# Kernel optimization log

Hardware: AMD Instinct MI355X
Metric: run time of the kernel (lower is better)

The kernel has to match this reference:

```python
import jax, jax.numpy as jnp
import numpy as np

B, N_ATOMS, D = 4, 100000, 64
F, G, A = 8, 20000, 3
H = 16


def setup_inputs() -> dict:
    key = jax.random.key(0)
    k1, k2, k3, k4 = jax.random.split(key, 4)
    atoms_embeddings = jax.random.normal(k1, (B, N_ATOMS, D), dtype=jnp.float32)
    grounding_indices = jax.random.randint(k2, (F, G, A), 0, N_ATOMS, dtype=jnp.int64)
    # Glorot-ish scaling so sigmoids don't saturate
    W1 = jax.random.normal(k3, (F, A * D, H), dtype=jnp.float32) / np.sqrt(A * D)
    b1 = jnp.zeros((F, H), dtype=jnp.float32)
    W2 = jax.random.normal(k4, (F, H, 1), dtype=jnp.float32) / np.sqrt(H)
    b2 = jnp.zeros((F, 1), dtype=jnp.float32)
    return {
        "atoms_embeddings": atoms_embeddings,
        "grounding_indices": grounding_indices,
        "W1": W1, "b1": b1, "W2": W2, "b2": b2,
    }


def reference(atoms_embeddings, grounding_indices, W1, b1, W2, b2):
    # Gather clique atom embeddings: [B, F, G, A, D]
    gathered = jnp.take(atoms_embeddings, grounding_indices, axis=1)
    # Fuse atoms of each clique: [B, F, G, A*D]
    Bsz = atoms_embeddings.shape[0]
    x = gathered.reshape(Bsz, F, G, A * gathered.shape[-1])
    # Per-formula 2-layer sigmoid MLP (dropout is identity in inference)
    h = jax.nn.sigmoid(jnp.einsum('bfgk,fkh->bfgh', x, W1) + b1[None, :, None, :])
    o = jax.nn.sigmoid(jnp.einsum('bfgh,fho->bfgo', h, W2) + b2[None, :, None, :])
    # Squeeze last dim and concat formulas along last axis: [B, F*G]
    return o[..., 0].reshape(Bsz, F * G)
```

## Files before the change

kernel.cpp:

```cpp
#include <hip/hip_runtime.h>

#define B_      4
#define N_ATOMS 100000
#define D_      64
#define F_      8
#define G_      20000
#define A_      3
#define H_      16
#define AD_     (A_ * D_)
#define BLOCK   256
#define GPB     64
#define BSTRIDE ((size_t)N_ATOMS * D_)

#define FMA16(x1, wr)                                            \
    {                                                            \
        const float4 w0 = (wr)[0], w1v = (wr)[1],                \
                     w2v = (wr)[2], w3v = (wr)[3];               \
        h[0]  = fmaf((x1), w0.x,  h[0]);                         \
        h[1]  = fmaf((x1), w0.y,  h[1]);                         \
        h[2]  = fmaf((x1), w0.z,  h[2]);                         \
        h[3]  = fmaf((x1), w0.w,  h[3]);                         \
        h[4]  = fmaf((x1), w1v.x, h[4]);                         \
        h[5]  = fmaf((x1), w1v.y, h[5]);                         \
        h[6]  = fmaf((x1), w1v.z, h[6]);                         \
        h[7]  = fmaf((x1), w1v.w, h[7]);                         \
        h[8]  = fmaf((x1), w2v.x, h[8]);                         \
        h[9]  = fmaf((x1), w2v.y, h[9]);                         \
        h[10] = fmaf((x1), w2v.z, h[10]);                        \
        h[11] = fmaf((x1), w2v.w, h[11]);                        \
        h[12] = fmaf((x1), w3v.x, h[12]);                        \
        h[13] = fmaf((x1), w3v.y, h[13]);                        \
        h[14] = fmaf((x1), w3v.z, h[14]);                        \
        h[15] = fmaf((x1), w3v.w, h[15]);                        \
    }

#define COMPUTE_SEG4(bufv, kbase)                                            \
    {                                                                        \
        _Pragma("unroll")                                                    \
        for (int k4 = 0; k4 < 4; ++k4) {                                     \
            const float4 xv = (bufv)[k4];                                    \
            const float4* wr =                                               \
                (const float4*)&w1s[((kbase) + k4 * 4) * H_];                \
            FMA16(xv.x, wr + 0);                                             \
            FMA16(xv.y, wr + 4);                                             \
            FMA16(xv.z, wr + 8);                                             \
            FMA16(xv.w, wr + 12);                                            \
        }                                                                    \
    }

__global__ __launch_bounds__(BLOCK)
void cliques_mlp_kernel(const float* __restrict__ atoms,
                        const int*   __restrict__ gi,
                        const float* __restrict__ W1,
                        const float* __restrict__ b1,
                        const float* __restrict__ W2,
                        const float* __restrict__ b2,
                        float* __restrict__ out)
{
    __shared__ __align__(16) float w1s[AD_ * H_];
    __shared__ float b1s[H_];
    __shared__ float w2s[H_];
    __shared__ float b2s_s;
    __shared__ int   is64_s;

    const int f   = blockIdx.y;
    const int tid = threadIdx.x;

    {
        const float4* src = (const float4*)(W1 + (size_t)f * AD_ * H_);
        float4*       dst = (float4*)w1s;
        #pragma unroll
        for (int i = 0; i < (AD_ * H_) / 4; i += BLOCK)
            dst[i + tid] = src[i + tid];
    }
    if (tid < H_) {
        b1s[tid] = b1[f * H_ + tid];
        w2s[tid] = W2[f * H_ + tid];
    }
    if (tid == 0) {
        b2s_s = b2[f];
        unsigned ored = 0u;
        const unsigned* u = (const unsigned*)gi;
        #pragma unroll
        for (int i = 0; i < 32; ++i) ored |= u[2 * i + 1];
        is64_s = (ored == 0u) ? 1 : 0;
    }
    __syncthreads();

    const int lane = tid & 63;
    const int b    = tid >> 6;
    const int g    = blockIdx.x * GPB + lane;
    if (g >= G_) return;

    const long long eidx = ((long long)f * G_ + g) * A_;
    int i0, i1, i2;
    if (is64_s) {
        i0 = gi[2 * (eidx + 0)];
        i1 = gi[2 * (eidx + 1)];
        i2 = gi[2 * (eidx + 2)];
    } else {
        i0 = gi[eidx + 0];
        i1 = gi[eidx + 1];
        i2 = gi[eidx + 2];
    }

    const float* base = atoms + (size_t)b * BSTRIDE;
    const float4* rp0 = (const float4*)(base + (size_t)i0 * D_);
    const float4* rp1 = (const float4*)(base + (size_t)i1 * D_);
    const float4* rp2 = (const float4*)(base + (size_t)i2 * D_);

    float h[H_];
    #pragma unroll
    for (int j = 0; j < H_; ++j) h[j] = b1s[j];

    float4 xa[4], xb[4];
    #pragma unroll
    for (int i = 0; i < 4; ++i) xa[i] = rp0[i];

    #pragma unroll 1
    for (int sp = 0; sp < 6; ++sp) {
        {
            const int so = 2 * sp + 1;
            const int ro = so >> 2, qo = so & 3;
            const float4* po = (ro == 0) ? rp0 : (ro == 1) ? rp1 : rp2;
            po += qo * 4;
            #pragma unroll
            for (int i = 0; i < 4; ++i) xb[i] = po[i];
        }
        COMPUTE_SEG4(xa, (2 * sp) * 16);

        if (sp < 5) {
            const int se = 2 * sp + 2;
            const int re = se >> 2, qe = se & 3;
            const float4* pe = (re == 0) ? rp0 : (re == 1) ? rp1 : rp2;
            pe += qe * 4;
            #pragma unroll
            for (int i = 0; i < 4; ++i) xa[i] = pe[i];
        }
        COMPUTE_SEG4(xb, (2 * sp + 1) * 16);
    }

    float o = b2s_s;
    #pragma unroll
    for (int j = 0; j < H_; ++j) {
        const float s = 1.0f / (1.0f + __expf(-h[j]));
        o = fmaf(s, w2s[j], o);
    }
    o = 1.0f / (1.0f + __expf(-o));
    out[(size_t)b * (F_ * G_) + (size_t)f * G_ + g] = o;
}

extern "C" void kernel_launch(void* const* d_in, const int* in_sizes, int n_in,
                              void* d_out, int out_size, void* d_ws, size_t ws_size,
                              hipStream_t stream) {
    const float* atoms = (const float*)d_in[0];
    const int*   gi    = (const int*)d_in[1];
    const float* W1    = (const float*)d_in[2];
    const float* b1    = (const float*)d_in[3];
    const float* W2    = (const float*)d_in[4];
    const float* b2    = (const float*)d_in[5];
    float*       out   = (float*)d_out;

    dim3 grid((G_ + GPB - 1) / GPB, F_);
    cliques_mlp_kernel<<<grid, dim3(BLOCK), 0, stream>>>(atoms, gi, W1, b1, W2, b2, out);
}
```

Before: 260.9 us.

## Pre-convert atom embeddings to bf16 table and gather half-width rows

Adds a pre-pass that converts the whole fp32 atom embedding tensor to bf16 in workspace. The MLP kernel then gathers bf16 rows, halving the bytes fetched per random gather, and unpacks them to fp32 before the FMAs. This costs an extra full read of the embeddings (about 100MB) plus a 50MB write on every call, and it lowers input precision. If the workspace is too small, the code falls back to the original fp32 kernel.

Measured after the change: 481.3 us. +84.5%, slower.

```diff
diff --git a/kernel.cpp b/kernel.cpp
--- a/kernel.cpp
+++ b/kernel.cpp
@@ -11,6 +11,7 @@
 #define BLOCK   256
 #define GPB     64
 #define BSTRIDE ((size_t)N_ATOMS * D_)
+#define NTOT    ((size_t)B_ * N_ATOMS * D_)
 
 #define FMA16(x1, wr)                                            \
     {                                                            \
@@ -34,6 +35,148 @@
         h[15] = fmaf((x1), w3v.w, h[15]);                        \
     }
 
+#define PAIR_BF16(u, kk)                                                     \
+    {                                                                        \
+        const float4* wr = (const float4*)&w1s[(size_t)(kk) * H_];           \
+        const float flo = __uint_as_float((u) << 16);                        \
+        const float fhi = __uint_as_float((u) & 0xffff0000u);                \
+        FMA16(flo, wr);                                                      \
+        FMA16(fhi, wr + 4);                                                  \
+    }
+
+#define COMPUTE_SEG_BF16(bufv, kbase)                                        \
+    {                                                                        \
+        _Pragma("unroll")                                                    \
+        for (int q = 0; q < 4; ++q) {                                        \
+            const uint4 uv = (bufv)[q];                                      \
+            PAIR_BF16(uv.x, (kbase) + q * 8 + 0);                            \
+            PAIR_BF16(uv.y, (kbase) + q * 8 + 2);                            \
+            PAIR_BF16(uv.z, (kbase) + q * 8 + 4);                            \
+            PAIR_BF16(uv.w, (kbase) + q * 8 + 6);                            \
+        }                                                                    \
+    }
+
+__device__ __forceinline__ unsigned int bf16_rn(float x) {
+    unsigned int u = __float_as_uint(x);
+    return (u + 0x7fffu + ((u >> 16) & 1u)) >> 16;
+}
+
+__global__ __launch_bounds__(256)
+void convert_bf16_kernel(const float* __restrict__ atoms,
+                         unsigned short* __restrict__ tab) {
+    const size_t i = ((size_t)blockIdx.x * 256 + threadIdx.x) * 8;
+    if (i >= NTOT) return;
+    const float4 a = *(const float4*)(atoms + i);
+    const float4 b = *(const float4*)(atoms + i + 4);
+    uint4 o;
+    o.x = bf16_rn(a.x) | (bf16_rn(a.y) << 16);
+    o.y = bf16_rn(a.z) | (bf16_rn(a.w) << 16);
+    o.z = bf16_rn(b.x) | (bf16_rn(b.y) << 16);
+    o.w = bf16_rn(b.z) | (bf16_rn(b.w) << 16);
+    *(uint4*)(tab + i) = o;
+}
+
+__global__ __launch_bounds__(BLOCK)
+void cliques_mlp_bf16_kernel(const unsigned short* __restrict__ tab,
+                             const int*   __restrict__ gi,
+                             const float* __restrict__ W1,
+                             const float* __restrict__ b1,
+                             const float* __restrict__ W2,
+                             const float* __restrict__ b2,
+                             float* __restrict__ out) {
+    __shared__ __align__(16) float w1s[AD_ * H_];
+    __shared__ float b1s[H_];
+    __shared__ float w2s[H_];
+    __shared__ float b2s_s;
+    __shared__ int   is64_s;
+
+    const int f   = blockIdx.y;
+    const int tid = threadIdx.x;
+
+    {
+        const float4* src = (const float4*)(W1 + (size_t)f * AD_ * H_);
+        float4*       dst = (float4*)w1s;
+        #pragma unroll
+        for (int i = 0; i < (AD_ * H_) / 4; i += BLOCK)
+            dst[i + tid] = src[i + tid];
+    }
+    if (tid < H_) {
+        b1s[tid] = b1[f * H_ + tid];
+        w2s[tid] = W2[f * H_ + tid];
+    }
+    if (tid == 0) {
+        b2s_s = b2[f];
+        unsigned ored = 0u;
+        const unsigned* u = (const unsigned*)gi;
+        #pragma unroll
+        for (int i = 0; i < 32; ++i) ored |= u[2 * i + 1];
+        is64_s = (ored == 0u) ? 1 : 0;
+    }
+    __syncthreads();
+
+    const int lane = tid & 63;
+    const int b    = tid >> 6;
+    const int g    = blockIdx.x * GPB + lane;
+    if (g >= G_) return;
+
+    const long long eidx = ((long long)f * G_ + g) * A_;
+    int i0, i1, i2;
+    if (is64_s) {
+        i0 = gi[2 * (eidx + 0)];
+        i1 = gi[2 * (eidx + 1)];
+        i2 = gi[2 * (eidx + 2)];
+    } else {
+        i0 = gi[eidx + 0];
+        i1 = gi[eidx + 1];
+        i2 = gi[eidx + 2];
+    }
+
+    const unsigned short* base = tab + (size_t)b * BSTRIDE;
+    const uint4* rp0 = (const uint4*)(base + (size_t)i0 * D_);
+    const uint4* rp1 = (const uint4*)(base + (size_t)i1 * D_);
+    const uint4* rp2 = (const uint4*)(base + (size_t)i2 * D_);
+
+    float h[H_];
+    #pragma unroll
+    for (int j = 0; j < H_; ++j) h[j] = b1s[j];
+
+    uint4 xa[4], xb[4];
+    #pragma unroll
+    for (int i = 0; i < 4; ++i) xa[i] = rp0[i];
+
+    #pragma unroll 1
+    for (int sp = 0; sp < 3; ++sp) {
+        {
+            const int so = 2 * sp + 1;
+            const int ro = so >> 1, ho = so & 1;
+            const uint4* po = (ro == 0) ? rp0 : (ro == 1) ? rp1 : rp2;
+            po += ho * 4;
+            #pragma unroll
+            for (int i = 0; i < 4; ++i) xb[i] = po[i];
+        }
+        COMPUTE_SEG_BF16(xa, (2 * sp) * 32);
+
+        if (sp < 2) {
+            const int se = 2 * sp + 2;
+            const int re = se >> 1, he = se & 1;
+            const uint4* pe = (re == 0) ? rp0 : (re == 1) ? rp1 : rp2;
+            pe += he * 4;
+            #pragma unroll
+            for (int i = 0; i < 4; ++i) xa[i] = pe[i];
+        }
+        COMPUTE_SEG_BF16(xb, (2 * sp + 1) * 32);
+    }
+
+    float o = b2s_s;
+    #pragma unroll
+    for (int j = 0; j < H_; ++j) {
+        const float s = 1.0f / (1.0f + __expf(-h[j]));
+        o = fmaf(s, w2s[j], o);
+    }
+    o = 1.0f / (1.0f + __expf(-o));
+    out[(size_t)b * (F_ * G_) + (size_t)f * G_ + g] = o;
+}
+
 #define COMPUTE_SEG4(bufv, kbase)                                            \
     {                                                                        \
         _Pragma("unroll")                                                    \
@@ -55,8 +198,7 @@
                         const float* __restrict__ b1,
                         const float* __restrict__ W2,
                         const float* __restrict__ b2,
-                        float* __restrict__ out)
-{
+                        float* __restrict__ out) {
     __shared__ __align__(16) float w1s[AD_ * H_];
     __shared__ float b1s[H_];
     __shared__ float w2s[H_];
@@ -162,5 +304,15 @@
     float*       out   = (float*)d_out;
 
     dim3 grid((G_ + GPB - 1) / GPB, F_);
-    cliques_mlp_kernel<<<grid, dim3(BLOCK), 0, stream>>>(atoms, gi, W1, b1, W2, b2, out);
-}
+
+    if (ws_size >= NTOT * sizeof(unsigned short)) {
+        unsigned short* tab = (unsigned short*)d_ws;
+        const int conv_blocks = (int)((NTOT / 8 + 255) / 256);
+        convert_bf16_kernel<<<conv_blocks, 256, 0, stream>>>(atoms, tab);
+        cliques_mlp_bf16_kernel<<<grid, dim3(BLOCK), 0, stream>>>(
+            tab, gi, W1, b1, W2, b2, out);
+    } else {
+        cliques_mlp_kernel<<<grid, dim3(BLOCK), 0, stream>>>(
+            atoms, gi, W1, b1, W2, b2, out);
+    }
+}
```

## Split each clique's K-reduction across two lanes with shuffle combine

Applied to the files above, without the earlier changes.

Each clique's 192-long dot-product reduction is now split between two adjacent lanes, each handling 96 elements (six 16-float segments spanning the atom rows). Partial hidden sums are combined with a lane-xor shuffle, and only the even lane writes the output. Blocks cover half as many cliques, which doubles the grid and the number of threads. This raises memory-level parallelism for the gathered loads and shortens per-thread latency chains, at the cost of extra shuffles and duplicated sigmoid work.

Result: slower. 306.8 us (+17.6%).

```diff
diff --git a/kernel.cpp b/kernel.cpp
--- a/kernel.cpp
+++ b/kernel.cpp
@@ -9,7 +9,7 @@
 #define H_      16
 #define AD_     (A_ * D_)
 #define BLOCK   256
-#define GPB     64
+#define GPB     32
 #define BSTRIDE ((size_t)N_ATOMS * D_)
 
 #define FMA16(x1, wr)                                            \
@@ -89,56 +89,65 @@
 
     const int lane = tid & 63;
     const int b    = tid >> 6;
-    const int g    = blockIdx.x * GPB + lane;
-    if (g >= G_) return;
+    const int c    = lane >> 1;
+    const int hh   = lane & 1;
+    const int g    = blockIdx.x * GPB + c;
 
-    const long long eidx = ((long long)f * G_ + g) * A_;
-    int i0, i1, i2;
+    const long long e3 = ((long long)f * G_ + g) * A_;
+    int idx_lo, idx_hi;
     if (is64_s) {
-        i0 = gi[2 * (eidx + 0)];
-        i1 = gi[2 * (eidx + 1)];
-        i2 = gi[2 * (eidx + 2)];
+        idx_lo = gi[2 * (e3 + hh)];
+        idx_hi = gi[2 * (e3 + 1 + hh)];
     } else {
-        i0 = gi[eidx + 0];
-        i1 = gi[eidx + 1];
-        i2 = gi[eidx + 2];
+        idx_lo = gi[e3 + hh];
+        idx_hi = gi[e3 + 1 + hh];
     }
 
     const float* base = atoms + (size_t)b * BSTRIDE;
-    const float4* rp0 = (const float4*)(base + (size_t)i0 * D_);
-    const float4* rp1 = (const float4*)(base + (size_t)i1 * D_);
-    const float4* rp2 = (const float4*)(base + (size_t)i2 * D_);
+    const float4* rp_lo = (const float4*)(base + (size_t)idx_lo * D_);
+    const float4* rp_hi = (const float4*)(base + (size_t)idx_hi * D_);
+
+    const int hh2    = 2 * hh;
+    const int thresh = 4 - hh2;
+#define SEGPTR(s) ( (((s) < thresh) ? rp_lo : rp_hi) +                       \
+                    ((((s) < thresh) ? ((s) + hh2) : ((s) - thresh)) * 4) )
+
+    const int khh = hh * 6 * 16;
 
     float h[H_];
     #pragma unroll
     for (int j = 0; j < H_; ++j) h[j] = b1s[j];
 
     float4 xa[4], xb[4];
-    #pragma unroll
-    for (int i = 0; i < 4; ++i) xa[i] = rp0[i];
+    {
+        const float4* p0 = SEGPTR(0);
+        #pragma unroll
+        for (int i = 0; i < 4; ++i) xa[i] = p0[i];
+    }
 
     #pragma unroll 1
-    for (int sp = 0; sp < 6; ++sp) {
+    for (int sp = 0; sp < 3; ++sp) {
         {
             const int so = 2 * sp + 1;
-            const int ro = so >> 2, qo = so & 3;
-            const float4* po = (ro == 0) ? rp0 : (ro == 1) ? rp1 : rp2;
-            po += qo * 4;
+            const float4* po = SEGPTR(so);
             #pragma unroll
             for (int i = 0; i < 4; ++i) xb[i] = po[i];
         }
-        COMPUTE_SEG4(xa, (2 * sp) * 16);
+        COMPUTE_SEG4(xa, khh + (2 * sp) * 16);
 
-        if (sp < 5) {
+        if (sp < 2) {
             const int se = 2 * sp + 2;
-            const int re = se >> 2, qe = se & 3;
-            const float4* pe = (re == 0) ? rp0 : (re == 1) ? rp1 : rp2;
-            pe += qe * 4;
+            const float4* pe = SEGPTR(se);
             #pragma unroll
             for (int i = 0; i < 4; ++i) xa[i] = pe[i];
         }
-        COMPUTE_SEG4(xb, (2 * sp + 1) * 16);
+        COMPUTE_SEG4(xb, khh + (2 * sp + 1) * 16);
     }
+#undef SEGPTR
+
+    #pragma unroll
+    for (int j = 0; j < H_; ++j)
+        h[j] += __shfl_xor(h[j], 1);
 
     float o = b2s_s;
     #pragma unroll
@@ -147,7 +156,8 @@
         o = fmaf(s, w2s[j], o);
     }
     o = 1.0f / (1.0f + __expf(-o));
-    out[(size_t)b * (F_ * G_) + (size_t)f * G_ + g] = o;
+    if (hh == 0)
+        out[(size_t)b * (F_ * G_) + (size_t)f * G_ + g] = o;
 }
 
 extern "C" void kernel_launch(void* const* d_in, const int* in_sizes, int n_in,
@@ -161,6 +171,6 @@
     const float* b2    = (const float*)d_in[5];
     float*       out   = (float*)d_out;
 
-    dim3 grid((G_ + GPB - 1) / GPB, F_);
+    dim3 grid(G_ / GPB, F_);
     cliques_mlp_kernel<<<grid, dim3(BLOCK), 0, stream>>>(atoms, gi, W1, b1, W2, b2, out);
 }
```
